# Performance work log

Hardware: AMD Instinct MI355X
Metric: run time of the kernel (lower is better)

Reference implementation:

```python
import jax, jax.numpy as jnp
import numpy as np

DIM = 512
HEADS = 8
DIM_HEAD = 64
HIDDEN = HEADS * DIM_HEAD  # 512
SCALE = DIM_HEAD ** -0.5
EPS = 1e-12  # F.normalize default eps


def rms_norm(x, g):
    # F.normalize over channel dim (dim=1), then * g * sqrt(C)
    c = x.shape[1]
    norm = jnp.sqrt(jnp.sum(x * x, axis=1, keepdims=True))
    return x / jnp.maximum(norm, EPS) * g * (c ** 0.5)


def setup_inputs() -> dict:
    key = jax.random.key(0)
    ks = jax.random.split(key, 6)
    b, h, w = 16, 64, 64
    x = jax.random.normal(ks[0], (b, DIM, h, w), dtype=jnp.float32)
    g1 = jnp.ones((1, DIM, 1, 1), dtype=jnp.float32)
    # 1x1 conv weights stored as (out_ch, in_ch)
    Wqkv = jax.random.normal(ks[1], (HIDDEN * 3, DIM), dtype=jnp.float32) * (DIM ** -0.5)
    Wout = jax.random.normal(ks[2], (DIM, HIDDEN), dtype=jnp.float32) * (HIDDEN ** -0.5)
    bout = jax.random.normal(ks[3], (DIM,), dtype=jnp.float32) * 0.01
    g2 = jnp.ones((1, DIM, 1, 1), dtype=jnp.float32)
    return {"x": x, "g1": g1, "Wqkv": Wqkv, "Wout": Wout, "bout": bout, "g2": g2}


def reference(x, g1, Wqkv, Wout, bout, g2):
    b, c, h, w = x.shape
    n = h * w
    xn = rms_norm(x, g1)
    # 1x1 conv == channel matmul
    qkv = jnp.einsum('oc,bchw->bohw', Wqkv, xn)  # (b, 3*hidden, h, w)
    qkv = qkv.reshape(b, 3, HEADS, DIM_HEAD, n)
    q, k, v = qkv[:, 0], qkv[:, 1], qkv[:, 2]  # (b, heads, d, n)
    q = jax.nn.softmax(q, axis=-2) * SCALE      # softmax over feature dim
    k = jax.nn.softmax(k, axis=-1)               # softmax over spatial dim
    context = jnp.einsum('bhdn,bhen->bhde', k, v)  # (b,h,d,e) small
    out = jnp.einsum('bhde,bhdn->bhen', context, q)  # (b,h,e,n)
    out = out.reshape(b, HIDDEN, h, w)
    out = jnp.einsum('oc,bchw->bohw', Wout, out) + bout[None, :, None, None]
    return rms_norm(out, g2)
```

## Files before the change

kernel.cpp:

```cpp
#include <hip/hip_runtime.h>
#include <hip/hip_bf16.h>
#include <math.h>

#define B_ 16
#define C_ 512
#define N_ 4096
#define NCOL (B_ * N_)

typedef short bf16x8 __attribute__((ext_vector_type(8)));
typedef ushort ushort8_t __attribute__((ext_vector_type(8)));
typedef float f32x4 __attribute__((ext_vector_type(4)));

__device__ __forceinline__ ushort f2bf(float f) {
    unsigned u = __float_as_uint(f);
    unsigned r = (u + 0x7FFFu + ((u >> 16) & 1u)) >> 16;
    return (ushort)r;
}
__device__ __forceinline__ float bf2f(ushort u) {
    return __uint_as_float((unsigned)u << 16);
}
__device__ __forceinline__ void gload_lds16(const void* g, void* l) {
    __builtin_amdgcn_global_load_lds(
        (const __attribute__((address_space(1))) unsigned int*)g,
        (__attribute__((address_space(3))) unsigned int*)l, 16, 0, 0);
}

__global__ __launch_bounds__(256) void wprep_k(const float* __restrict__ W,
                                               const float* __restrict__ g,
                                               ushort* __restrict__ Wb, int nvec)
{
    int i = blockIdx.x * 256 + threadIdx.x;
    if (i >= nvec) return;
    float4 wv = reinterpret_cast<const float4*>(W)[i];
    if (g) {
        const float4 gv = *reinterpret_cast<const float4*>(g + ((i * 4) & 511));
        wv.x *= gv.x; wv.y *= gv.y; wv.z *= gv.z; wv.w *= gv.w;
    }
    ushort4 u;
    u.x = f2bf(wv.x); u.y = f2bf(wv.y); u.z = f2bf(wv.z); u.w = f2bf(wv.w);
    reinterpret_cast<ushort4*>(Wb)[i] = u;
}

__global__ __launch_bounds__(256) void transpose_k(const float* __restrict__ X,
                                                   ushort* __restrict__ Xt,
                                                   float* __restrict__ csq1)
{
    __shared__ float t[64][65];
    __shared__ float sq[4][64];
    const int b = blockIdx.z, n0 = blockIdx.x * 64, c0 = blockIdx.y * 64;
    const int tid = threadIdx.x;
    const int tx = tid & 63, ty = tid >> 6;
    const float* xp = X + ((size_t)b * C_ + c0) * N_ + n0;
    float local = 0.f;
    #pragma unroll
    for (int i = 0; i < 16; ++i) {
        float v = xp[(size_t)(ty + 4 * i) * N_ + tx];
        t[ty + 4 * i][tx] = v;
        local += v * v;
    }
    sq[ty][tx] = local;
    __syncthreads();
    #pragma unroll
    for (int i = 0; i < 4; ++i) {
        int nl = (tid >> 4) + i * 16;
        int cl = (tid & 15) * 4;
        ushort4 u;
        u.x = f2bf(t[cl + 0][nl]);
        u.y = f2bf(t[cl + 1][nl]);
        u.z = f2bf(t[cl + 2][nl]);
        u.w = f2bf(t[cl + 3][nl]);
        *reinterpret_cast<ushort4*>(Xt + ((size_t)b * N_ + n0 + nl) * 512 + c0 + cl) = u;
    }
    if (tid < 64)
        csq1[(size_t)blockIdx.y * NCOL + (size_t)b * N_ + n0 + tid] =
            sq[0][tid] + sq[1][tid] + sq[2][tid] + sq[3][tid];
}

__global__ __launch_bounds__(256) void rs1_reduce_k(const float* __restrict__ csq1,
                                                    float* __restrict__ rs1)
{
    int col = blockIdx.x * 256 + threadIdx.x;
    float s = 0.f;
    #pragma unroll
    for (int j = 0; j < 8; ++j) s += csq1[(size_t)j * NCOL + col];
    rs1[col] = 22.627416998f / fmaxf(sqrtf(s), 1e-12f);
}

__global__ __launch_bounds__(512, 2)
void mfma_gemm(const ushort* __restrict__ A, const ushort* __restrict__ Bt,
               const float* __restrict__ rs1,
               ushort* __restrict__ qT, ushort* __restrict__ kd,
               ushort* __restrict__ vd)
{
    __shared__ __align__(16) char lds[2][2][32768];
    const int b  = blockIdx.z;
    const int n0 = blockIdx.x * 256;
    const int m0 = blockIdx.y * 256;
    const int tid = threadIdx.x;
    const int w = tid >> 6, l = tid & 63;
    const int wm = w >> 2, wn = w & 3;
    const int lq = l >> 4, lr = l & 15;
    const ushort* Bb = Bt + (size_t)b * N_ * 512;

    f32x4 acc[8][4];
    #pragma unroll
    for (int i = 0; i < 8; ++i)
        #pragma unroll
        for (int j = 0; j < 4; ++j)
            #pragma unroll
            for (int r = 0; r < 4; ++r) acc[i][j][r] = 0.f;

#define STAGE_STEP(t, i)                                                      \
    do {                                                                      \
        const int kb_ = (t) * 128;                                            \
        const int idx_ = (i) * 512 + tid;                                     \
        const int r_ = idx_ >> 3;                                             \
        const int ch_ = (idx_ & 7) ^ (r_ & 7);                                \
        gload_lds16((const char*)A + (size_t)(m0 + r_) * 1024 + kb_ + ch_ * 16,\
                    &lds[(t) & 1][0][idx_ * 16]);                             \
        gload_lds16((const char*)Bb + (size_t)(n0 + r_) * 1024 + kb_ + ch_ * 16,\
                    &lds[(t) & 1][1][idx_ * 16]);                             \
    } while (0)

    #pragma unroll
    for (int i = 0; i < 4; ++i) STAGE_STEP(0, i);

    bf16x8 bfr[4];
    #pragma unroll 2
    for (int t = 0; t < 8; ++t) {
        const char* As = lds[t & 1][0];
        const char* Bs = lds[t & 1][1];
        #pragma unroll
        for (int ph = 0; ph < 4; ++ph) {
            const int kk = ph >> 1, mg = ph & 1;
            bf16x8 af[4];
            if (ph != 0) {
                #pragma unroll
                for (int m2 = 0; m2 < 4; ++m2) {
                    int ra = wm * 128 + (mg * 4 + m2) * 16 + lr;
                    int ch = (kk * 4 + lq) ^ (ra & 7);
                    af[m2] = *(const bf16x8*)(As + ra * 128 + ch * 16);
                }
                if (mg == 0) {
                    #pragma unroll
                    for (int nf = 0; nf < 4; ++nf) {
                        int rb = wn * 64 + nf * 16 + lr;
                        int ch = (kk * 4 + lq) ^ (rb & 7);
                        bfr[nf] = *(const bf16x8*)(Bs + rb * 128 + ch * 16);
                    }
                }
            }
            if (t < 7) STAGE_STEP(t + 1, ph);
            if (ph == 0) {
                if (t < 7) { asm volatile("s_waitcnt vmcnt(2)" ::: "memory"); }
                else       { asm volatile("s_waitcnt vmcnt(0)" ::: "memory"); }
            }
            __builtin_amdgcn_s_barrier();
            if (ph == 0) {
                #pragma unroll
                for (int m2 = 0; m2 < 4; ++m2) {
                    int ra = wm * 128 + m2 * 16 + lr;
                    int ch = lq ^ (ra & 7);
                    af[m2] = *(const bf16x8*)(As + ra * 128 + ch * 16);
                }
                #pragma unroll
                for (int nf = 0; nf < 4; ++nf) {
                    int rb = wn * 64 + nf * 16 + lr;
                    int ch = lq ^ (rb & 7);
                    bfr[nf] = *(const bf16x8*)(Bs + rb * 128 + ch * 16);
                }
            }
            asm volatile("s_waitcnt lgkmcnt(0)" ::: "memory");
            __builtin_amdgcn_sched_barrier(0);
            __builtin_amdgcn_s_setprio(1);
            #pragma unroll
            for (int m2 = 0; m2 < 4; ++m2)
                #pragma unroll
                for (int nf = 0; nf < 4; ++nf)
                    acc[mg * 4 + m2][nf] = __builtin_amdgcn_mfma_f32_16x16x32_bf16(
                        af[m2], bfr[nf], acc[mg * 4 + m2][nf], 0, 0, 0);
            __builtin_amdgcn_s_setprio(0);
            __builtin_amdgcn_s_barrier();
        }
    }
#undef STAGE_STEP

    const int part = m0 >> 9;
    const int mloc = (m0 & 511) + wm * 128;
    const int nbase = n0 + wn * 64;
    if (part == 0) {
        #pragma unroll
        for (int hg = 0; hg < 2; ++hg) {
            const int head = (mloc >> 6) + hg;
            #pragma unroll
            for (int nf = 0; nf < 4; ++nf) {
                const int n = nbase + nf * 16 + lr;
                const float sc = rs1[(size_t)b * N_ + n];
                float v[4][4];
                float mx = -1e30f;
                #pragma unroll
                for (int m2 = 0; m2 < 4; ++m2)
                    #pragma unroll
                    for (int r = 0; r < 4; ++r) {
                        v[m2][r] = acc[hg * 4 + m2][nf][r] * sc;
                        mx = fmaxf(mx, v[m2][r]);
                    }
                mx = fmaxf(mx, __shfl_xor(mx, 16));
                mx = fmaxf(mx, __shfl_xor(mx, 32));
                float s = 0.f;
                #pragma unroll
                for (int m2 = 0; m2 < 4; ++m2)
                    #pragma unroll
                    for (int r = 0; r < 4; ++r) {
                        v[m2][r] = __expf(v[m2][r] - mx);
                        s += v[m2][r];
                    }
                s += __shfl_xor(s, 16);
                s += __shfl_xor(s, 32);
                const float r8 = 0.125f / s;
                ushort* qp = qT + (((size_t)b * 8 + head) * N_ + n) * 64;
                #pragma unroll
                for (int m2 = 0; m2 < 4; ++m2) {
                    ushort4 u;
                    u.x = f2bf(v[m2][0] * r8);
                    u.y = f2bf(v[m2][1] * r8);
                    u.z = f2bf(v[m2][2] * r8);
                    u.w = f2bf(v[m2][3] * r8);
                    *reinterpret_cast<ushort4*>(qp + m2 * 16 + lq * 4) = u;
                }
            }
        }
    } else {
        ushort* dst = (part == 1) ? kd : vd;
        #pragma unroll
        for (int nf = 0; nf < 4; ++nf) {
            const int n = nbase + nf * 16 + lr;
            const float sc = rs1[(size_t)b * N_ + n];
            #pragma unroll
            for (int mf = 0; mf < 8; ++mf) {
                const int o = mloc + mf * 16 + lq * 4;
                #pragma unroll
                for (int r = 0; r < 4; ++r)
                    dst[((size_t)b * 512 + o + r) * N_ + n] =
                        f2bf(acc[mf][nf][r] * sc);
            }
        }
    }
}

__global__ __launch_bounds__(512, 2)
void gemm2_k(const ushort* __restrict__ A,
             const ushort* __restrict__ Bt,
             const float* __restrict__ bias,
             const float* __restrict__ g2,
             float* __restrict__ outp)
{
    __shared__ __align__(16) ushort As[512 * 64];
    __shared__ __align__(16) ushort Bs[128 * 64];
    const int b  = blockIdx.y;
    const int n0 = blockIdx.x * 128;
    const int tid = threadIdx.x;
    const int w = tid >> 6, l = tid & 63;
    const int lq = l >> 4, lr = l & 15;
    const ushort* Bb = Bt + (size_t)b * N_ * 512;

    f32x4 acc[4][8];
    #pragma unroll
    for (int i = 0; i < 4; ++i)
        #pragma unroll
        for (int j = 0; j < 8; ++j)
            #pragma unroll
            for (int r = 0; r < 4; ++r) acc[i][j][r] = 0.f;

    for (int k0 = 0; k0 < 512; k0 += 64) {
        #pragma unroll
        for (int i = 0; i < 8; ++i) {
            int base = i * 512 + w * 64;
            int idx = base + l;
            int r = idx >> 3, ch = (idx & 7) ^ (r & 7);
            gload_lds16((const char*)A + (size_t)r * 1024 + k0 * 2 + ch * 16,
                        (char*)As + (size_t)base * 16);
        }
        #pragma unroll
        for (int i = 0; i < 2; ++i) {
            int base = i * 512 + w * 64;
            int idx = base + l;
            int r = idx >> 3, ch = (idx & 7) ^ (r & 7);
            gload_lds16((const char*)Bb + (size_t)(n0 + r) * 1024 + k0 * 2 + ch * 16,
                        (char*)Bs + (size_t)base * 16);
        }
        __syncthreads();
        #pragma unroll
        for (int kk = 0; kk < 2; ++kk) {
            bf16x8 af[4], bfr[8];
            #pragma unroll
            for (int mf = 0; mf < 4; ++mf) {
                int ra = w * 64 + mf * 16 + lr;
                int ch = (kk * 4 + lq) ^ (ra & 7);
                af[mf] = *(const bf16x8*)((const char*)As + ra * 128 + ch * 16);
            }
            #pragma unroll
            for (int nf = 0; nf < 8; ++nf) {
                int rb = nf * 16 + lr;
                int ch = (kk * 4 + lq) ^ (rb & 7);
                bfr[nf] = *(const bf16x8*)((const char*)Bs + rb * 128 + ch * 16);
            }
            #pragma unroll
            for (int mf = 0; mf < 4; ++mf)
                #pragma unroll
                for (int nf = 0; nf < 8; ++nf)
                    acc[mf][nf] = __builtin_amdgcn_mfma_f32_16x16x32_bf16(
                        af[mf], bfr[nf], acc[mf][nf], 0, 0, 0);
        }
        __syncthreads();
    }

    float4 bv[4], g2v[4];
    #pragma unroll
    for (int mf = 0; mf < 4; ++mf) {
        bv[mf]  = *reinterpret_cast<const float4*>(bias + w * 64 + mf * 16 + lq * 4);
        g2v[mf] = *reinterpret_cast<const float4*>(g2   + w * 64 + mf * 16 + lq * 4);
    }
    float csq[8] = {};
    #pragma unroll
    for (int mf = 0; mf < 4; ++mf)
        #pragma unroll
        for (int nf = 0; nf < 8; ++nf)
            #pragma unroll
            for (int r = 0; r < 4; ++r) {
                float wv = acc[mf][nf][r] + ((const float*)&bv[mf])[r];
                acc[mf][nf][r] = wv;
                csq[nf] += wv * wv;
            }
    #pragma unroll
    for (int nf = 0; nf < 8; ++nf) {
        csq[nf] += __shfl_xor(csq[nf], 16);
        csq[nf] += __shfl_xor(csq[nf], 32);
    }
    float* red  = (float*)As;
    float* rs2s = red + 1024;
    if (lq == 0) {
        #pragma unroll
        for (int nf = 0; nf < 8; ++nf)
            red[w * 128 + nf * 16 + lr] = csq[nf];
    }
    __syncthreads();
    if (tid < 128) {
        float s = 0.f;
        #pragma unroll
        for (int j = 0; j < 8; ++j) s += red[j * 128 + tid];
        rs2s[tid] = 22.627416998f / fmaxf(sqrtf(s), 1e-12f);
    }
    __syncthreads();
    #pragma unroll
    for (int nf = 0; nf < 8; ++nf) {
        const float rsv = rs2s[nf * 16 + lr];
        const int n = n0 + nf * 16 + lr;
        #pragma unroll
        for (int mf = 0; mf < 4; ++mf) {
            const int o = w * 64 + mf * 16 + lq * 4;
            float* p = outp + ((size_t)b * 512 + o) * N_ + n;
            #pragma unroll
            for (int r = 0; r < 4; ++r)
                p[(size_t)r * N_] = acc[mf][nf][r] * rsv * ((const float*)&g2v[mf])[r];
        }
    }
}

__global__ __launch_bounds__(256) void rowstat_k(const ushort* __restrict__ kk,
                                                 float* __restrict__ rowm,
                                                 float* __restrict__ rowr)
{
    const int row = blockIdx.x * 4 + (threadIdx.x >> 6);
    const int lane = threadIdx.x & 63;
    const ushort* p = kk + (size_t)row * N_;
    float vals[64];
    #pragma unroll
    for (int j = 0; j < 8; ++j) {
        ushort8_t u = *reinterpret_cast<const ushort8_t*>(p + lane * 8 + j * 512);
        #pragma unroll
        for (int t = 0; t < 8; ++t) vals[j * 8 + t] = bf2f(u[t]);
    }
    float mx = -1e30f;
    #pragma unroll
    for (int i = 0; i < 64; ++i) mx = fmaxf(mx, vals[i]);
    #pragma unroll
    for (int o = 32; o >= 1; o >>= 1) mx = fmaxf(mx, __shfl_xor(mx, o));
    float s = 0.f;
    #pragma unroll
    for (int i = 0; i < 64; ++i) s += __expf(vals[i] - mx);
    #pragma unroll
    for (int o = 32; o >= 1; o >>= 1) s += __shfl_xor(s, o);
    if (lane == 0) { rowm[row] = mx; rowr[row] = 1.f / s; }
}

__global__ __launch_bounds__(256) void ctx_k(const ushort* __restrict__ kk,
                                             const ushort* __restrict__ vv,
                                             const float* __restrict__ rowm,
                                             const float* __restrict__ rowr,
                                             float* __restrict__ ctxp)
{
    const int bh = blockIdx.x, chunk = blockIdx.y;
    const ushort* kp = kk + (size_t)bh * 64 * N_;
    const ushort* vp = vv + (size_t)bh * 64 * N_;
    __shared__ __align__(16) ushort kx[64 * 128];
    __shared__ __align__(16) ushort vx[64 * 128];
    __shared__ float rm[64];
    const int tid = threadIdx.x;
    const int w = tid >> 6, l = tid & 63;
    const int lq = l >> 4, lr = l & 15;
    const int we = w >> 1, wd = w & 1;
    if (tid < 64) rm[tid] = rowm[(size_t)bh * 64 + tid];
    __syncthreads();

    f32x4 acc[2][2];
    #pragma unroll
    for (int i = 0; i < 2; ++i)
        #pragma unroll
        for (int j = 0; j < 2; ++j)
            #pragma unroll
            for (int r = 0; r < 4; ++r) acc[i][j][r] = 0.f;

    for (int s = 0; s < 8; ++s) {
        const int n0 = chunk * 1024 + s * 128;
        #pragma unroll
        for (int i = 0; i < 4; ++i) {
            int idx = i * 256 + tid;
            int row = idx >> 4;
            int ch  = (idx & 15) ^ (row & 15);
            gload_lds16((const char*)(vp + (size_t)row * N_ + n0 + ch * 8),
                        (char*)vx + idx * 16);
        }
        #pragma unroll
        for (int i = 0; i < 4; ++i) {
            int idx = i * 256 + tid;
            int row = idx >> 4;
            int ch  = idx & 15;
            ushort8_t u = *reinterpret_cast<const ushort8_t*>(
                kp + (size_t)row * N_ + n0 + ch * 8);
            float m_ = rm[row];
            ushort8_t o;
            #pragma unroll
            for (int t = 0; t < 8; ++t) o[t] = f2bf(__expf(bf2f(u[t]) - m_));
            *(ushort8_t*)((char*)kx + (row * 16 + (ch ^ (row & 15))) * 16) = o;
        }
        __syncthreads();
        #pragma unroll
        for (int k2 = 0; k2 < 4; ++k2) {
            bf16x8 af[2], bfr[2];
            #pragma unroll
            for (int i = 0; i < 2; ++i) {
                int re = we * 32 + i * 16 + lr;
                int cha = (k2 * 4 + lq) ^ (re & 15);
                af[i] = *(const bf16x8*)((const char*)vx + (re * 16 + cha) * 16);
                int rd = wd * 32 + i * 16 + lr;
                int chb = (k2 * 4 + lq) ^ (rd & 15);
                bfr[i] = *(const bf16x8*)((const char*)kx + (rd * 16 + chb) * 16);
            }
            #pragma unroll
            for (int i = 0; i < 2; ++i)
                #pragma unroll
                for (int j = 0; j < 2; ++j)
                    acc[i][j] = __builtin_amdgcn_mfma_f32_16x16x32_bf16(
                        af[i], bfr[j], acc[i][j], 0, 0, 0);
        }
        __syncthreads();
    }
    float* cbase = ctxp + ((size_t)bh * 4 + chunk) * 4096;
    #pragma unroll
    for (int j = 0; j < 2; ++j) {
        const int d = wd * 32 + j * 16 + lr;
        const float rr = rowr[(size_t)bh * 64 + d];
        #pragma unroll
        for (int i = 0; i < 2; ++i) {
            const int e = we * 32 + i * 16 + lq * 4;
            #pragma unroll
            for (int r = 0; r < 4; ++r)
                cbase[(size_t)(e + r) * 64 + d] = acc[i][j][r] * rr;
        }
    }
}

__global__ __launch_bounds__(256) void attn_k(const float* __restrict__ ctxp,
                                              const ushort* __restrict__ qT,
                                              ushort* __restrict__ at2)
{
    const int bh = blockIdx.y;
    const int n0 = blockIdx.x * 256;
    const int b = bh >> 3, h = bh & 7;
    __shared__ __align__(16) ushort qx[256 * 64];
    __shared__ __align__(16) ushort cx[64 * 64];
    const int tid = threadIdx.x;
    const int w = tid >> 6, l = tid & 63;
    const int lq = l >> 4, lr = l & 15;
    const ushort* qp = qT + ((size_t)bh * N_ + n0) * 64;

    #pragma unroll
    for (int i = 0; i < 8; ++i) {
        int idx = i * 256 + tid;
        int row = idx >> 3;
        int ch  = (idx & 7) ^ (row & 7);
        gload_lds16((const char*)(qp + (size_t)row * 64 + ch * 8),
                    (char*)qx + idx * 16);
    }
    {
        const float* cp = ctxp + (size_t)bh * 4 * 4096;
        const int e = tid >> 2, db = (tid & 3) * 16;
        float vs[16];
        #pragma unroll
        for (int t = 0; t < 4; ++t) {
            float4 a0 = *(const float4*)(cp + e * 64 + db + t * 4);
            float4 a1 = *(const float4*)(cp + 4096 + e * 64 + db + t * 4);
            float4 a2 = *(const float4*)(cp + 8192 + e * 64 + db + t * 4);
            float4 a3 = *(const float4*)(cp + 12288 + e * 64 + db + t * 4);
            vs[t * 4 + 0] = a0.x + a1.x + a2.x + a3.x;
            vs[t * 4 + 1] = a0.y + a1.y + a2.y + a3.y;
            vs[t * 4 + 2] = a0.z + a1.z + a2.z + a3.z;
            vs[t * 4 + 3] = a0.w + a1.w + a2.w + a3.w;
        }
        ushort8_t o0, o1;
        #pragma unroll
        for (int t = 0; t < 8; ++t) { o0[t] = f2bf(vs[t]); o1[t] = f2bf(vs[8 + t]); }
        const int c0 = (db >> 3) ^ (e & 7);
        const int c1 = ((db >> 3) + 1) ^ (e & 7);
        *(ushort8_t*)((char*)cx + (e * 8 + c0) * 16) = o0;
        *(ushort8_t*)((char*)cx + (e * 8 + c1) * 16) = o1;
    }
    __syncthreads();

    f32x4 acc[4][4];
    #pragma unroll
    for (int i = 0; i < 4; ++i)
        #pragma unroll
        for (int j = 0; j < 4; ++j)
            #pragma unroll
            for (int r = 0; r < 4; ++r) acc[i][j][r] = 0.f;

    #pragma unroll
    for (int k2 = 0; k2 < 2; ++k2) {
        bf16x8 af[4], bfr[4];
        #pragma unroll
        for (int et = 0; et < 4; ++et) {
            int re = et * 16 + lr;
            int ch = (k2 * 4 + lq) ^ (re & 7);
            af[et] = *(const bf16x8*)((const char*)cx + (re * 8 + ch) * 16);
        }
        #pragma unroll
        for (int nt = 0; nt < 4; ++nt) {
            int rn = w * 64 + nt * 16 + lr;
            int ch = (k2 * 4 + lq) ^ (rn & 7);
            bfr[nt] = *(const bf16x8*)((const char*)qx + (rn * 8 + ch) * 16);
        }
        #pragma unroll
        for (int et = 0; et < 4; ++et)
            #pragma unroll
            for (int nt = 0; nt < 4; ++nt)
                acc[et][nt] = __builtin_amdgcn_mfma_f32_16x16x32_bf16(
                    af[et], bfr[nt], acc[et][nt], 0, 0, 0);
    }
    #pragma unroll
    for (int nt = 0; nt < 4; ++nt) {
        const int n = n0 + w * 64 + nt * 16 + lr;
        ushort* op = at2 + ((size_t)b * N_ + n) * 512 + h * 64;
        #pragma unroll
        for (int et = 0; et < 4; ++et) {
            ushort4 u;
            u.x = f2bf(acc[et][nt][0]);
            u.y = f2bf(acc[et][nt][1]);
            u.z = f2bf(acc[et][nt][2]);
            u.w = f2bf(acc[et][nt][3]);
            *reinterpret_cast<ushort4*>(op + et * 16 + lq * 4) = u;
        }
    }
}

extern "C" void kernel_launch(void* const* d_in, const int* in_sizes, int n_in,
                              void* d_out, int out_size, void* d_ws, size_t ws_size,
                              hipStream_t stream)
{
    const float* x    = (const float*)d_in[0];
    const float* g1   = (const float*)d_in[1];
    const float* Wqkv = (const float*)d_in[2];
    const float* Wout = (const float*)d_in[3];
    const float* bout = (const float*)d_in[4];
    const float* g2   = (const float*)d_in[5];
    float* out = (float*)d_out;

    char* wsb = (char*)d_ws;
    ushort* qbuf  = (ushort*)wsb;
    float*  csq1  = (float*)wsb;
    ushort* kbuf  = (ushort*)(wsb + ((size_t)64 << 20));
    ushort* vbuf  = (ushort*)(wsb + ((size_t)128 << 20));
    ushort* Xt    = (ushort*)(wsb + ((size_t)192 << 20));
    float*  ctxp  = (float*)Xt;
    float*  rowm  = (float*)(wsb + ((size_t)200 << 20));
    float*  rowr  = rowm + 8192;
    char*   tail  = wsb + ((size_t)256 << 20);
    ushort* Wqkvb = (ushort*)tail;
    ushort* Woutb = (ushort*)(tail + (size_t)1536 * 512 * 2);
    float*  rs1   = (float*)(tail + (size_t)1536 * 512 * 2 + (size_t)512 * 512 * 2);
    ushort* at2   = kbuf;

    wprep_k<<<768, 256, 0, stream>>>(Wqkv, g1, Wqkvb, 1536 * 512 / 4);
    wprep_k<<<256, 256, 0, stream>>>(Wout, nullptr, Woutb, 512 * 512 / 4);
    transpose_k<<<dim3(64, 8, 16), 256, 0, stream>>>(x, Xt, csq1);
    rs1_reduce_k<<<256, 256, 0, stream>>>(csq1, rs1);
    mfma_gemm<<<dim3(16, 6, B_), 512, 0, stream>>>(Wqkvb, Xt, rs1,
                                                   qbuf, kbuf, vbuf);
    rowstat_k<<<2048, 256, 0, stream>>>(kbuf, rowm, rowr);
    ctx_k<<<dim3(B_ * 8, 4), 256, 0, stream>>>(kbuf, vbuf, rowm, rowr, ctxp);
    attn_k<<<dim3(N_ / 256, B_ * 8), 256, 0, stream>>>(ctxp, qbuf, at2);
    gemm2_k<<<dim3(32, B_), 512, 0, stream>>>(Woutb, at2, bout, g2, out);
}
```

Measured before the change: 339.6 us.

## Fuse attention output into output-projection GEMM, keeping attended tile in LDS

Replaces the attn_k plus gemm2_k pair with a small ctxsum kernel that pre-reduces context partials to bf16, and a fused kernel. The fused kernel computes context·q per head for a 64-column tile, holds the result in LDS, and runs the Wout projection with bias and RMS norm directly on it. This removes the global write and re-read of the 64 MB intermediate at2 buffer. In exchange the tile shrinks from 128 to 64 columns with one block per CU and 128 KB of LDS, so Wout is streamed twice as often and occupancy is lower.

```diff
diff --git a/kernel.cpp b/kernel.cpp
--- a/kernel.cpp
+++ b/kernel.cpp
@@ -248,125 +248,6 @@
     }
 }
 
-__global__ __launch_bounds__(512, 2)
-void gemm2_k(const ushort* __restrict__ A,
-             const ushort* __restrict__ Bt,
-             const float* __restrict__ bias,
-             const float* __restrict__ g2,
-             float* __restrict__ outp)
-{
-    __shared__ __align__(16) ushort As[512 * 64];
-    __shared__ __align__(16) ushort Bs[128 * 64];
-    const int b  = blockIdx.y;
-    const int n0 = blockIdx.x * 128;
-    const int tid = threadIdx.x;
-    const int w = tid >> 6, l = tid & 63;
-    const int lq = l >> 4, lr = l & 15;
-    const ushort* Bb = Bt + (size_t)b * N_ * 512;
-
-    f32x4 acc[4][8];
-    #pragma unroll
-    for (int i = 0; i < 4; ++i)
-        #pragma unroll
-        for (int j = 0; j < 8; ++j)
-            #pragma unroll
-            for (int r = 0; r < 4; ++r) acc[i][j][r] = 0.f;
-
-    for (int k0 = 0; k0 < 512; k0 += 64) {
-        #pragma unroll
-        for (int i = 0; i < 8; ++i) {
-            int base = i * 512 + w * 64;
-            int idx = base + l;
-            int r = idx >> 3, ch = (idx & 7) ^ (r & 7);
-            gload_lds16((const char*)A + (size_t)r * 1024 + k0 * 2 + ch * 16,
-                        (char*)As + (size_t)base * 16);
-        }
-        #pragma unroll
-        for (int i = 0; i < 2; ++i) {
-            int base = i * 512 + w * 64;
-            int idx = base + l;
-            int r = idx >> 3, ch = (idx & 7) ^ (r & 7);
-            gload_lds16((const char*)Bb + (size_t)(n0 + r) * 1024 + k0 * 2 + ch * 16,
-                        (char*)Bs + (size_t)base * 16);
-        }
-        __syncthreads();
-        #pragma unroll
-        for (int kk = 0; kk < 2; ++kk) {
-            bf16x8 af[4], bfr[8];
-            #pragma unroll
-            for (int mf = 0; mf < 4; ++mf) {
-                int ra = w * 64 + mf * 16 + lr;
-                int ch = (kk * 4 + lq) ^ (ra & 7);
-                af[mf] = *(const bf16x8*)((const char*)As + ra * 128 + ch * 16);
-            }
-            #pragma unroll
-            for (int nf = 0; nf < 8; ++nf) {
-                int rb = nf * 16 + lr;
-                int ch = (kk * 4 + lq) ^ (rb & 7);
-                bfr[nf] = *(const bf16x8*)((const char*)Bs + rb * 128 + ch * 16);
-            }
-            #pragma unroll
-            for (int mf = 0; mf < 4; ++mf)
-                #pragma unroll
-                for (int nf = 0; nf < 8; ++nf)
-                    acc[mf][nf] = __builtin_amdgcn_mfma_f32_16x16x32_bf16(
-                        af[mf], bfr[nf], acc[mf][nf], 0, 0, 0);
-        }
-        __syncthreads();
-    }
-
-    float4 bv[4], g2v[4];
-    #pragma unroll
-    for (int mf = 0; mf < 4; ++mf) {
-        bv[mf]  = *reinterpret_cast<const float4*>(bias + w * 64 + mf * 16 + lq * 4);
-        g2v[mf] = *reinterpret_cast<const float4*>(g2   + w * 64 + mf * 16 + lq * 4);
-    }
-    float csq[8] = {};
-    #pragma unroll
-    for (int mf = 0; mf < 4; ++mf)
-        #pragma unroll
-        for (int nf = 0; nf < 8; ++nf)
-            #pragma unroll
-            for (int r = 0; r < 4; ++r) {
-                float wv = acc[mf][nf][r] + ((const float*)&bv[mf])[r];
-                acc[mf][nf][r] = wv;
-                csq[nf] += wv * wv;
-            }
-    #pragma unroll
-    for (int nf = 0; nf < 8; ++nf) {
-        csq[nf] += __shfl_xor(csq[nf], 16);
-        csq[nf] += __shfl_xor(csq[nf], 32);
-    }
-    float* red  = (float*)As;
-    float* rs2s = red + 1024;
-    if (lq == 0) {
-        #pragma unroll
-        for (int nf = 0; nf < 8; ++nf)
-            red[w * 128 + nf * 16 + lr] = csq[nf];
-    }
-    __syncthreads();
-    if (tid < 128) {
-        float s = 0.f;
-        #pragma unroll
-        for (int j = 0; j < 8; ++j) s += red[j * 128 + tid];
-        rs2s[tid] = 22.627416998f / fmaxf(sqrtf(s), 1e-12f);
-    }
-    __syncthreads();
-    #pragma unroll
-    for (int nf = 0; nf < 8; ++nf) {
-        const float rsv = rs2s[nf * 16 + lr];
-        const int n = n0 + nf * 16 + lr;
-        #pragma unroll
-        for (int mf = 0; mf < 4; ++mf) {
-            const int o = w * 64 + mf * 16 + lq * 4;
-            float* p = outp + ((size_t)b * 512 + o) * N_ + n;
-            #pragma unroll
-            for (int r = 0; r < 4; ++r)
-                p[(size_t)r * N_] = acc[mf][nf][r] * rsv * ((const float*)&g2v[mf])[r];
-        }
-    }
-}
-
 __global__ __launch_bounds__(256) void rowstat_k(const ushort* __restrict__ kk,
                                                  float* __restrict__ rowm,
                                                  float* __restrict__ rowr)
@@ -481,51 +362,94 @@
     }
 }
 
-__global__ __launch_bounds__(256) void attn_k(const float* __restrict__ ctxp,
-                                              const ushort* __restrict__ qT,
-                                              ushort* __restrict__ at2)
-{
-    const int bh = blockIdx.y;
-    const int n0 = blockIdx.x * 256;
-    const int b = bh >> 3, h = bh & 7;
-    __shared__ __align__(16) ushort qx[256 * 64];
-    __shared__ __align__(16) ushort cx[64 * 64];
+__global__ __launch_bounds__(256) void ctxsum_k(const float* __restrict__ ctxp,
+                                                ushort* __restrict__ ctxb)
+{
+    int i4 = blockIdx.x * 256 + threadIdx.x;
+    int bh = i4 >> 10;
+    int off = (i4 & 1023) * 4;
+    const float* cp = ctxp + (size_t)bh * 16384 + off;
+    float4 a0 = *(const float4*)cp;
+    float4 a1 = *(const float4*)(cp + 4096);
+    float4 a2 = *(const float4*)(cp + 8192);
+    float4 a3 = *(const float4*)(cp + 12288);
+    ushort4 u;
+    u.x = f2bf(a0.x + a1.x + a2.x + a3.x);
+    u.y = f2bf(a0.y + a1.y + a2.y + a3.y);
+    u.z = f2bf(a0.z + a1.z + a2.z + a3.z);
+    u.w = f2bf(a0.w + a1.w + a2.w + a3.w);
+    *reinterpret_cast<ushort4*>(ctxb + (size_t)bh * 4096 + off) = u;
+}
+
+__global__ __launch_bounds__(512, 1)
+void gemm2f_k(const ushort* __restrict__ A,
+              const ushort* __restrict__ qT,
+              const ushort* __restrict__ ctxb,
+              const float* __restrict__ bias,
+              const float* __restrict__ g2,
+              float* __restrict__ outp)
+{
+    __shared__ __align__(16) char As[65536];
+    __shared__ __align__(16) char Bs[65536];
+    const int b  = blockIdx.y;
+    const int n0 = blockIdx.x * 64;
     const int tid = threadIdx.x;
     const int w = tid >> 6, l = tid & 63;
     const int lq = l >> 4, lr = l & 15;
-    const ushort* qp = qT + ((size_t)bh * N_ + n0) * 64;
-
-    #pragma unroll
-    for (int i = 0; i < 8; ++i) {
-        int idx = i * 256 + tid;
-        int row = idx >> 3;
-        int ch  = (idx & 7) ^ (row & 7);
-        gload_lds16((const char*)(qp + (size_t)row * 64 + ch * 8),
-                    (char*)qx + idx * 16);
-    }
+
     {
-        const float* cp = ctxp + (size_t)bh * 4 * 4096;
-        const int e = tid >> 2, db = (tid & 3) * 16;
-        float vs[16];
-        #pragma unroll
-        for (int t = 0; t < 4; ++t) {
-            float4 a0 = *(const float4*)(cp + e * 64 + db + t * 4);
-            float4 a1 = *(const float4*)(cp + 4096 + e * 64 + db + t * 4);
-            float4 a2 = *(const float4*)(cp + 8192 + e * 64 + db + t * 4);
-            float4 a3 = *(const float4*)(cp + 12288 + e * 64 + db + t * 4);
-            vs[t * 4 + 0] = a0.x + a1.x + a2.x + a3.x;
-            vs[t * 4 + 1] = a0.y + a1.y + a2.y + a3.y;
-            vs[t * 4 + 2] = a0.z + a1.z + a2.z + a3.z;
-            vs[t * 4 + 3] = a0.w + a1.w + a2.w + a3.w;
-        }
-        ushort8_t o0, o1;
-        #pragma unroll
-        for (int t = 0; t < 8; ++t) { o0[t] = f2bf(vs[t]); o1[t] = f2bf(vs[8 + t]); }
-        const int c0 = (db >> 3) ^ (e & 7);
-        const int c1 = ((db >> 3) + 1) ^ (e & 7);
-        *(ushort8_t*)((char*)cx + (e * 8 + c0) * 16) = o0;
-        *(ushort8_t*)((char*)cx + (e * 8 + c1) * 16) = o1;
-    }
+        const int n = tid >> 3;
+        const int j = tid & 7;
+        const int ch = j ^ (n & 7);
+        #pragma unroll
+        for (int h = 0; h < 8; ++h) {
+            gload_lds16(qT + (((size_t)b * 8 + h) * N_ + n0 + n) * 64 + ch * 8,
+                        As + h * 8192 + tid * 16);
+            gload_lds16(ctxb + (((size_t)b * 8 + h) * 64 + n) * 64 + ch * 8,
+                        Bs + h * 8192 + tid * 16);
+        }
+    }
+    __syncthreads();
+
+    bf16x8 paf[4][2], pbf[4][2];
+    #pragma unroll
+    for (int mf = 0; mf < 4; ++mf)
+        #pragma unroll
+        for (int k2 = 0; k2 < 2; ++k2) {
+            int rr = mf * 16 + lr;
+            int sl = (k2 * 4 + lq) ^ (rr & 7);
+            paf[mf][k2] = *(const bf16x8*)(As + w * 8192 + rr * 128 + sl * 16);
+            pbf[mf][k2] = *(const bf16x8*)(Bs + w * 8192 + rr * 128 + sl * 16);
+        }
+    __syncthreads();
+
+    f32x4 pacc[4][4];
+    #pragma unroll
+    for (int i = 0; i < 4; ++i)
+        #pragma unroll
+        for (int j = 0; j < 4; ++j)
+            #pragma unroll
+            for (int r = 0; r < 4; ++r) pacc[i][j][r] = 0.f;
+    #pragma unroll
+    for (int k2 = 0; k2 < 2; ++k2)
+        #pragma unroll
+        for (int mf = 0; mf < 4; ++mf)
+            #pragma unroll
+            for (int nf = 0; nf < 4; ++nf)
+                pacc[mf][nf] = __builtin_amdgcn_mfma_f32_16x16x32_bf16(
+                    paf[mf][k2], pbf[nf][k2], pacc[mf][nf], 0, 0, 0);
+
+    #pragma unroll
+    for (int mf = 0; mf < 4; ++mf)
+        #pragma unroll
+        for (int nf = 0; nf < 4; ++nf)
+            #pragma unroll
+            for (int r = 0; r < 4; ++r) {
+                int n = mf * 16 + lq * 4 + r;
+                int c = w * 64 + nf * 16 + lr;
+                *(ushort*)(Bs + ((n * 1024 + c * 2) ^ ((n & 7) << 4))) =
+                    f2bf(pacc[mf][nf][r]);
+            }
     __syncthreads();
 
     f32x4 acc[4][4];
@@ -536,40 +460,89 @@
             #pragma unroll
             for (int r = 0; r < 4; ++r) acc[i][j][r] = 0.f;
 
-    #pragma unroll
-    for (int k2 = 0; k2 < 2; ++k2) {
-        bf16x8 af[4], bfr[4];
-        #pragma unroll
-        for (int et = 0; et < 4; ++et) {
-            int re = et * 16 + lr;
-            int ch = (k2 * 4 + lq) ^ (re & 7);
-            af[et] = *(const bf16x8*)((const char*)cx + (re * 8 + ch) * 16);
-        }
-        #pragma unroll
-        for (int nt = 0; nt < 4; ++nt) {
-            int rn = w * 64 + nt * 16 + lr;
-            int ch = (k2 * 4 + lq) ^ (rn & 7);
-            bfr[nt] = *(const bf16x8*)((const char*)qx + (rn * 8 + ch) * 16);
-        }
-        #pragma unroll
-        for (int et = 0; et < 4; ++et)
-            #pragma unroll
-            for (int nt = 0; nt < 4; ++nt)
-                acc[et][nt] = __builtin_amdgcn_mfma_f32_16x16x32_bf16(
-                    af[et], bfr[nt], acc[et][nt], 0, 0, 0);
-    }
-    #pragma unroll
-    for (int nt = 0; nt < 4; ++nt) {
-        const int n = n0 + w * 64 + nt * 16 + lr;
-        ushort* op = at2 + ((size_t)b * N_ + n) * 512 + h * 64;
-        #pragma unroll
-        for (int et = 0; et < 4; ++et) {
-            ushort4 u;
-            u.x = f2bf(acc[et][nt][0]);
-            u.y = f2bf(acc[et][nt][1]);
-            u.z = f2bf(acc[et][nt][2]);
-            u.w = f2bf(acc[et][nt][3]);
-            *reinterpret_cast<ushort4*>(op + et * 16 + lq * 4) = u;
+    for (int t = 0; t < 8; ++t) {
+        #pragma unroll
+        for (int jj = 0; jj < 8; ++jj) {
+            int idx = jj * 512 + tid;
+            int m = idx >> 3;
+            int ch = (idx & 7) ^ (m & 7);
+            gload_lds16((const char*)A + (size_t)m * 1024 + t * 128 + ch * 16,
+                        As + idx * 16);
+        }
+        __syncthreads();
+        #pragma unroll
+        for (int kk = 0; kk < 2; ++kk) {
+            bf16x8 af[4], bfv[4];
+            #pragma unroll
+            for (int mf = 0; mf < 4; ++mf) {
+                int m = w * 64 + mf * 16 + lr;
+                int sl = (kk * 4 + lq) ^ (m & 7);
+                af[mf] = *(const bf16x8*)(As + m * 128 + sl * 16);
+            }
+            #pragma unroll
+            for (int nf = 0; nf < 4; ++nf) {
+                int n = nf * 16 + lr;
+                int sl = (kk * 4 + lq) ^ (n & 7);
+                bfv[nf] = *(const bf16x8*)(Bs + n * 1024 + t * 128 + sl * 16);
+            }
+            #pragma unroll
+            for (int mf = 0; mf < 4; ++mf)
+                #pragma unroll
+                for (int nf = 0; nf < 4; ++nf)
+                    acc[mf][nf] = __builtin_amdgcn_mfma_f32_16x16x32_bf16(
+                        af[mf], bfv[nf], acc[mf][nf], 0, 0, 0);
+        }
+        __syncthreads();
+    }
+
+    float4 bv[4], gv[4];
+    #pragma unroll
+    for (int mf = 0; mf < 4; ++mf) {
+        bv[mf] = *reinterpret_cast<const float4*>(bias + w * 64 + mf * 16 + lq * 4);
+        gv[mf] = *reinterpret_cast<const float4*>(g2   + w * 64 + mf * 16 + lq * 4);
+    }
+    float csq[4] = {};
+    #pragma unroll
+    for (int mf = 0; mf < 4; ++mf)
+        #pragma unroll
+        for (int nf = 0; nf < 4; ++nf)
+            #pragma unroll
+            for (int r = 0; r < 4; ++r) {
+                float wv = acc[mf][nf][r] + ((const float*)&bv[mf])[r];
+                acc[mf][nf][r] = wv;
+                csq[nf] += wv * wv;
+            }
+    #pragma unroll
+    for (int nf = 0; nf < 4; ++nf) {
+        csq[nf] += __shfl_xor(csq[nf], 16);
+        csq[nf] += __shfl_xor(csq[nf], 32);
+    }
+    float* red  = (float*)As;
+    float* rs2s = red + 512;
+    if (lq == 0) {
+        #pragma unroll
+        for (int nf = 0; nf < 4; ++nf)
+            red[w * 64 + nf * 16 + lr] = csq[nf];
+    }
+    __syncthreads();
+    if (tid < 64) {
+        float s = 0.f;
+        #pragma unroll
+        for (int j = 0; j < 8; ++j) s += red[j * 64 + tid];
+        rs2s[tid] = 22.627416998f / fmaxf(sqrtf(s), 1e-12f);
+    }
+    __syncthreads();
+    #pragma unroll
+    for (int nf = 0; nf < 4; ++nf) {
+        const float rsv = rs2s[nf * 16 + lr];
+        const int n = n0 + nf * 16 + lr;
+        #pragma unroll
+        for (int mf = 0; mf < 4; ++mf) {
+            const int o = w * 64 + mf * 16 + lq * 4;
+            float* p = outp + ((size_t)b * 512 + o) * N_ + n;
+            #pragma unroll
+            for (int r = 0; r < 4; ++r)
+                p[(size_t)r * N_] = acc[mf][nf][r] * rsv * ((const float*)&gv[mf])[r];
         }
     }
 }
@@ -595,11 +568,11 @@
     float*  ctxp  = (float*)Xt;
     float*  rowm  = (float*)(wsb + ((size_t)200 << 20));
     float*  rowr  = rowm + 8192;
+    ushort* ctxb  = (ushort*)(wsb + ((size_t)201 << 20));
     char*   tail  = wsb + ((size_t)256 << 20);
     ushort* Wqkvb = (ushort*)tail;
     ushort* Woutb = (ushort*)(tail + (size_t)1536 * 512 * 2);
     float*  rs1   = (float*)(tail + (size_t)1536 * 512 * 2 + (size_t)512 * 512 * 2);
-    ushort* at2   = kbuf;
 
     wprep_k<<<768, 256, 0, stream>>>(Wqkv, g1, Wqkvb, 1536 * 512 / 4);
     wprep_k<<<256, 256, 0, stream>>>(Wout, nullptr, Woutb, 512 * 512 / 4);
@@ -609,6 +582,6 @@
                                                    qbuf, kbuf, vbuf);
     rowstat_k<<<2048, 256, 0, stream>>>(kbuf, rowm, rowr);
     ctx_k<<<dim3(B_ * 8, 4), 256, 0, stream>>>(kbuf, vbuf, rowm, rowr, ctxp);
-    attn_k<<<dim3(N_ / 256, B_ * 8), 256, 0, stream>>>(ctxp, qbuf, at2);
-    gemm2_k<<<dim3(32, B_), 512, 0, stream>>>(Woutb, at2, bout, g2, out);
-}
+    ctxsum_k<<<512, 256, 0, stream>>>(ctxp, ctxb);
+    gemm2f_k<<<dim3(64, B_), 512, 0, stream>>>(Woutb, qbuf, ctxb, bout, g2, out);
+}
```

Measured after the change: 332.7 us. -2.0%, faster.

## Fold attention context into per-batch output weights, removing attn_k pass

Applied to the files above, without the earlier changes.

Uses associativity to fold the per-head context matrix into the output projection: a small wcbuild kernel computes Wc[b] = Wout·blockdiag(context) per batch. gemm2 then multiplies Wc directly against the softmaxed q, which the QKV GEMM now writes in (b, n, hidden) layout. This removes the attn_k kernel and its read and write of a large intermediate. In exchange it adds a small per-batch weight-build kernel, more strided q stores, and an extra bf16 rounding of the combined weights.

```diff
diff --git a/kernel.cpp b/kernel.cpp
--- a/kernel.cpp
+++ b/kernel.cpp
@@ -89,7 +89,7 @@
 __global__ __launch_bounds__(512, 2)
 void mfma_gemm(const ushort* __restrict__ A, const ushort* __restrict__ Bt,
                const float* __restrict__ rs1,
-               ushort* __restrict__ qT, ushort* __restrict__ kd,
+               ushort* __restrict__ qT2, ushort* __restrict__ kd,
                ushort* __restrict__ vd)
 {
     __shared__ __align__(16) char lds[2][2][32768];
@@ -218,7 +218,7 @@
                 s += __shfl_xor(s, 16);
                 s += __shfl_xor(s, 32);
                 const float r8 = 0.125f / s;
-                ushort* qp = qT + (((size_t)b * 8 + head) * N_ + n) * 64;
+                ushort* qp = qT2 + ((size_t)b * N_ + n) * 512 + head * 64;
                 #pragma unroll
                 for (int m2 = 0; m2 < 4; ++m2) {
                     ushort4 u;
@@ -244,125 +244,6 @@
                     dst[((size_t)b * 512 + o + r) * N_ + n] =
                         f2bf(acc[mf][nf][r] * sc);
             }
-        }
-    }
-}
-
-__global__ __launch_bounds__(512, 2)
-void gemm2_k(const ushort* __restrict__ A,
-             const ushort* __restrict__ Bt,
-             const float* __restrict__ bias,
-             const float* __restrict__ g2,
-             float* __restrict__ outp)
-{
-    __shared__ __align__(16) ushort As[512 * 64];
-    __shared__ __align__(16) ushort Bs[128 * 64];
-    const int b  = blockIdx.y;
-    const int n0 = blockIdx.x * 128;
-    const int tid = threadIdx.x;
-    const int w = tid >> 6, l = tid & 63;
-    const int lq = l >> 4, lr = l & 15;
-    const ushort* Bb = Bt + (size_t)b * N_ * 512;
-
-    f32x4 acc[4][8];
-    #pragma unroll
-    for (int i = 0; i < 4; ++i)
-        #pragma unroll
-        for (int j = 0; j < 8; ++j)
-            #pragma unroll
-            for (int r = 0; r < 4; ++r) acc[i][j][r] = 0.f;
-
-    for (int k0 = 0; k0 < 512; k0 += 64) {
-        #pragma unroll
-        for (int i = 0; i < 8; ++i) {
-            int base = i * 512 + w * 64;
-            int idx = base + l;
-            int r = idx >> 3, ch = (idx & 7) ^ (r & 7);
-            gload_lds16((const char*)A + (size_t)r * 1024 + k0 * 2 + ch * 16,
-                        (char*)As + (size_t)base * 16);
-        }
-        #pragma unroll
-        for (int i = 0; i < 2; ++i) {
-            int base = i * 512 + w * 64;
-            int idx = base + l;
-            int r = idx >> 3, ch = (idx & 7) ^ (r & 7);
-            gload_lds16((const char*)Bb + (size_t)(n0 + r) * 1024 + k0 * 2 + ch * 16,
-                        (char*)Bs + (size_t)base * 16);
-        }
-        __syncthreads();
-        #pragma unroll
-        for (int kk = 0; kk < 2; ++kk) {
-            bf16x8 af[4], bfr[8];
-            #pragma unroll
-            for (int mf = 0; mf < 4; ++mf) {
-                int ra = w * 64 + mf * 16 + lr;
-                int ch = (kk * 4 + lq) ^ (ra & 7);
-                af[mf] = *(const bf16x8*)((const char*)As + ra * 128 + ch * 16);
-            }
-            #pragma unroll
-            for (int nf = 0; nf < 8; ++nf) {
-                int rb = nf * 16 + lr;
-                int ch = (kk * 4 + lq) ^ (rb & 7);
-                bfr[nf] = *(const bf16x8*)((const char*)Bs + rb * 128 + ch * 16);
-            }
-            #pragma unroll
-            for (int mf = 0; mf < 4; ++mf)
-                #pragma unroll
-                for (int nf = 0; nf < 8; ++nf)
-                    acc[mf][nf] = __builtin_amdgcn_mfma_f32_16x16x32_bf16(
-                        af[mf], bfr[nf], acc[mf][nf], 0, 0, 0);
-        }
-        __syncthreads();
-    }
-
-    float4 bv[4], g2v[4];
-    #pragma unroll
-    for (int mf = 0; mf < 4; ++mf) {
-        bv[mf]  = *reinterpret_cast<const float4*>(bias + w * 64 + mf * 16 + lq * 4);
-        g2v[mf] = *reinterpret_cast<const float4*>(g2   + w * 64 + mf * 16 + lq * 4);
-    }
-    float csq[8] = {};
-    #pragma unroll
-    for (int mf = 0; mf < 4; ++mf)
-        #pragma unroll
-        for (int nf = 0; nf < 8; ++nf)
-            #pragma unroll
-            for (int r = 0; r < 4; ++r) {
-                float wv = acc[mf][nf][r] + ((const float*)&bv[mf])[r];
-                acc[mf][nf][r] = wv;
-                csq[nf] += wv * wv;
-            }
-    #pragma unroll
-    for (int nf = 0; nf < 8; ++nf) {
-        csq[nf] += __shfl_xor(csq[nf], 16);
-        csq[nf] += __shfl_xor(csq[nf], 32);
-    }
-    float* red  = (float*)As;
-    float* rs2s = red + 1024;
-    if (lq == 0) {
-        #pragma unroll
-        for (int nf = 0; nf < 8; ++nf)
-            red[w * 128 + nf * 16 + lr] = csq[nf];
-    }
-    __syncthreads();
-    if (tid < 128) {
-        float s = 0.f;
-        #pragma unroll
-        for (int j = 0; j < 8; ++j) s += red[j * 128 + tid];
-        rs2s[tid] = 22.627416998f / fmaxf(sqrtf(s), 1e-12f);
-    }
-    __syncthreads();
-    #pragma unroll
-    for (int nf = 0; nf < 8; ++nf) {
-        const float rsv = rs2s[nf * 16 + lr];
-        const int n = n0 + nf * 16 + lr;
-        #pragma unroll
-        for (int mf = 0; mf < 4; ++mf) {
-            const int o = w * 64 + mf * 16 + lq * 4;
-            float* p = outp + ((size_t)b * 512 + o) * N_ + n;
-            #pragma unroll
-            for (int r = 0; r < 4; ++r)
-                p[(size_t)r * N_] = acc[mf][nf][r] * rsv * ((const float*)&g2v[mf])[r];
         }
     }
 }
@@ -473,58 +354,59 @@
         const float rr = rowr[(size_t)bh * 64 + d];
         #pragma unroll
         for (int i = 0; i < 2; ++i) {
-            const int e = we * 32 + i * 16 + lq * 4;
-            #pragma unroll
-            for (int r = 0; r < 4; ++r)
-                cbase[(size_t)(e + r) * 64 + d] = acc[i][j][r] * rr;
-        }
-    }
-}
-
-__global__ __launch_bounds__(256) void attn_k(const float* __restrict__ ctxp,
-                                              const ushort* __restrict__ qT,
-                                              ushort* __restrict__ at2)
-{
-    const int bh = blockIdx.y;
-    const int n0 = blockIdx.x * 256;
-    const int b = bh >> 3, h = bh & 7;
-    __shared__ __align__(16) ushort qx[256 * 64];
-    __shared__ __align__(16) ushort cx[64 * 64];
+            const int e0 = we * 32 + i * 16 + lq * 4;
+            float4 wv;
+            wv.x = acc[i][j][0] * rr;
+            wv.y = acc[i][j][1] * rr;
+            wv.z = acc[i][j][2] * rr;
+            wv.w = acc[i][j][3] * rr;
+            *reinterpret_cast<float4*>(cbase + (size_t)d * 64 + e0) = wv;
+        }
+    }
+}
+
+__global__ __launch_bounds__(256) void wcbuild_k(const ushort* __restrict__ Wb,
+                                                 const float* __restrict__ ctxp,
+                                                 ushort* __restrict__ Wc)
+{
+    const int oh = blockIdx.x, h = blockIdx.y, b = blockIdx.z;
+    const int bh = b * 8 + h;
+    __shared__ __align__(16) ushort ws[256 * 64];
+    __shared__ __align__(16) ushort cs[64 * 64];
     const int tid = threadIdx.x;
     const int w = tid >> 6, l = tid & 63;
     const int lq = l >> 4, lr = l & 15;
-    const ushort* qp = qT + ((size_t)bh * N_ + n0) * 64;
 
     #pragma unroll
     for (int i = 0; i < 8; ++i) {
         int idx = i * 256 + tid;
         int row = idx >> 3;
-        int ch  = (idx & 7) ^ (row & 7);
-        gload_lds16((const char*)(qp + (size_t)row * 64 + ch * 8),
-                    (char*)qx + idx * 16);
+        int ch = (idx & 7) ^ (row & 7);
+        gload_lds16(Wb + (size_t)(oh * 256 + row) * 512 + h * 64 + ch * 8,
+                    (char*)ws + idx * 16);
     }
     {
         const float* cp = ctxp + (size_t)bh * 4 * 4096;
-        const int e = tid >> 2, db = (tid & 3) * 16;
+        const int d = tid >> 2, eb = (tid & 3) * 16;
         float vs[16];
         #pragma unroll
-        for (int t = 0; t < 4; ++t) {
-            float4 a0 = *(const float4*)(cp + e * 64 + db + t * 4);
-            float4 a1 = *(const float4*)(cp + 4096 + e * 64 + db + t * 4);
-            float4 a2 = *(const float4*)(cp + 8192 + e * 64 + db + t * 4);
-            float4 a3 = *(const float4*)(cp + 12288 + e * 64 + db + t * 4);
-            vs[t * 4 + 0] = a0.x + a1.x + a2.x + a3.x;
-            vs[t * 4 + 1] = a0.y + a1.y + a2.y + a3.y;
-            vs[t * 4 + 2] = a0.z + a1.z + a2.z + a3.z;
-            vs[t * 4 + 3] = a0.w + a1.w + a2.w + a3.w;
+        for (int t4 = 0; t4 < 4; ++t4) {
+            float4 a0 = *(const float4*)(cp + d * 64 + eb + t4 * 4);
+            float4 a1 = *(const float4*)(cp + 4096 + d * 64 + eb + t4 * 4);
+            float4 a2 = *(const float4*)(cp + 8192 + d * 64 + eb + t4 * 4);
+            float4 a3 = *(const float4*)(cp + 12288 + d * 64 + eb + t4 * 4);
+            vs[t4 * 4 + 0] = a0.x + a1.x + a2.x + a3.x;
+            vs[t4 * 4 + 1] = a0.y + a1.y + a2.y + a3.y;
+            vs[t4 * 4 + 2] = a0.z + a1.z + a2.z + a3.z;
+            vs[t4 * 4 + 3] = a0.w + a1.w + a2.w + a3.w;
         }
         ushort8_t o0, o1;
         #pragma unroll
         for (int t = 0; t < 8; ++t) { o0[t] = f2bf(vs[t]); o1[t] = f2bf(vs[8 + t]); }
-        const int c0 = (db >> 3) ^ (e & 7);
-        const int c1 = ((db >> 3) + 1) ^ (e & 7);
-        *(ushort8_t*)((char*)cx + (e * 8 + c0) * 16) = o0;
-        *(ushort8_t*)((char*)cx + (e * 8 + c1) * 16) = o1;
+        const int c0 = (eb >> 3) ^ (d & 7);
+        const int c1 = ((eb >> 3) + 1) ^ (d & 7);
+        *(ushort8_t*)((char*)cs + (d * 8 + c0) * 16) = o0;
+        *(ushort8_t*)((char*)cs + (d * 8 + c1) * 16) = o1;
     }
     __syncthreads();
 
@@ -537,39 +419,156 @@
             for (int r = 0; r < 4; ++r) acc[i][j][r] = 0.f;
 
     #pragma unroll
-    for (int k2 = 0; k2 < 2; ++k2) {
+    for (int kk = 0; kk < 2; ++kk) {
         bf16x8 af[4], bfr[4];
         #pragma unroll
-        for (int et = 0; et < 4; ++et) {
-            int re = et * 16 + lr;
-            int ch = (k2 * 4 + lq) ^ (re & 7);
-            af[et] = *(const bf16x8*)((const char*)cx + (re * 8 + ch) * 16);
-        }
-        #pragma unroll
-        for (int nt = 0; nt < 4; ++nt) {
-            int rn = w * 64 + nt * 16 + lr;
-            int ch = (k2 * 4 + lq) ^ (rn & 7);
-            bfr[nt] = *(const bf16x8*)((const char*)qx + (rn * 8 + ch) * 16);
-        }
-        #pragma unroll
-        for (int et = 0; et < 4; ++et)
-            #pragma unroll
-            for (int nt = 0; nt < 4; ++nt)
-                acc[et][nt] = __builtin_amdgcn_mfma_f32_16x16x32_bf16(
-                    af[et], bfr[nt], acc[et][nt], 0, 0, 0);
-    }
-    #pragma unroll
-    for (int nt = 0; nt < 4; ++nt) {
-        const int n = n0 + w * 64 + nt * 16 + lr;
-        ushort* op = at2 + ((size_t)b * N_ + n) * 512 + h * 64;
-        #pragma unroll
-        for (int et = 0; et < 4; ++et) {
-            ushort4 u;
-            u.x = f2bf(acc[et][nt][0]);
-            u.y = f2bf(acc[et][nt][1]);
-            u.z = f2bf(acc[et][nt][2]);
-            u.w = f2bf(acc[et][nt][3]);
-            *reinterpret_cast<ushort4*>(op + et * 16 + lq * 4) = u;
+        for (int mf = 0; mf < 4; ++mf) {
+            int ra = w * 64 + mf * 16 + lr;
+            int ch = (kk * 4 + lq) ^ (ra & 7);
+            af[mf] = *(const bf16x8*)((const char*)ws + (ra * 8 + ch) * 16);
+        }
+        #pragma unroll
+        for (int nf = 0; nf < 4; ++nf) {
+            int rd = nf * 16 + lr;
+            int ch = (kk * 4 + lq) ^ (rd & 7);
+            bfr[nf] = *(const bf16x8*)((const char*)cs + (rd * 8 + ch) * 16);
+        }
+        #pragma unroll
+        for (int mf = 0; mf < 4; ++mf)
+            #pragma unroll
+            for (int nf = 0; nf < 4; ++nf)
+                acc[mf][nf] = __builtin_amdgcn_mfma_f32_16x16x32_bf16(
+                    af[mf], bfr[nf], acc[mf][nf], 0, 0, 0);
+    }
+
+    ushort* wp = Wc + (size_t)b * 262144 + h * 64;
+    #pragma unroll
+    for (int mf = 0; mf < 4; ++mf)
+        #pragma unroll
+        for (int r = 0; r < 4; ++r) {
+            const int o = oh * 256 + w * 64 + mf * 16 + lq * 4 + r;
+            #pragma unroll
+            for (int nf = 0; nf < 4; ++nf)
+                wp[(size_t)o * 512 + nf * 16 + lr] = f2bf(acc[mf][nf][r]);
+        }
+}
+
+__global__ __launch_bounds__(512, 2)
+void gemm2_k(const ushort* __restrict__ Wc,
+             const ushort* __restrict__ Bt,
+             const float* __restrict__ bias,
+             const float* __restrict__ g2,
+             float* __restrict__ outp)
+{
+    __shared__ __align__(16) ushort As[512 * 64];
+    __shared__ __align__(16) ushort Bs[128 * 64];
+    const int b  = blockIdx.y;
+    const int n0 = blockIdx.x * 128;
+    const int tid = threadIdx.x;
+    const int w = tid >> 6, l = tid & 63;
+    const int lq = l >> 4, lr = l & 15;
+    const ushort* A  = Wc + (size_t)b * 262144;
+    const ushort* Bb = Bt + (size_t)b * N_ * 512;
+
+    f32x4 acc[4][8];
+    #pragma unroll
+    for (int i = 0; i < 4; ++i)
+        #pragma unroll
+        for (int j = 0; j < 8; ++j)
+            #pragma unroll
+            for (int r = 0; r < 4; ++r) acc[i][j][r] = 0.f;
+
+    for (int k0 = 0; k0 < 512; k0 += 64) {
+        #pragma unroll
+        for (int i = 0; i < 8; ++i) {
+            int base = i * 512 + w * 64;
+            int idx = base + l;
+            int r = idx >> 3, ch = (idx & 7) ^ (r & 7);
+            gload_lds16((const char*)A + (size_t)r * 1024 + k0 * 2 + ch * 16,
+                        (char*)As + (size_t)base * 16);
+        }
+        #pragma unroll
+        for (int i = 0; i < 2; ++i) {
+            int base = i * 512 + w * 64;
+            int idx = base + l;
+            int r = idx >> 3, ch = (idx & 7) ^ (r & 7);
+            gload_lds16((const char*)Bb + (size_t)(n0 + r) * 1024 + k0 * 2 + ch * 16,
+                        (char*)Bs + (size_t)base * 16);
+        }
+        __syncthreads();
+        #pragma unroll
+        for (int kk = 0; kk < 2; ++kk) {
+            bf16x8 af[4], bfv[8];
+            #pragma unroll
+            for (int mf = 0; mf < 4; ++mf) {
+                int ra = w * 64 + mf * 16 + lr;
+                int ch = (kk * 4 + lq) ^ (ra & 7);
+                af[mf] = *(const bf16x8*)((const char*)As + ra * 128 + ch * 16);
+            }
+            #pragma unroll
+            for (int nf = 0; nf < 8; ++nf) {
+                int rb = nf * 16 + lr;
+                int ch = (kk * 4 + lq) ^ (rb & 7);
+                bfv[nf] = *(const bf16x8*)((const char*)Bs + rb * 128 + ch * 16);
+            }
+            #pragma unroll
+            for (int mf = 0; mf < 4; ++mf)
+                #pragma unroll
+                for (int nf = 0; nf < 8; ++nf)
+                    acc[mf][nf] = __builtin_amdgcn_mfma_f32_16x16x32_bf16(
+                        af[mf], bfv[nf], acc[mf][nf], 0, 0, 0);
+        }
+        __syncthreads();
+    }
+
+    float4 bv[4], g2v[4];
+    #pragma unroll
+    for (int mf = 0; mf < 4; ++mf) {
+        bv[mf]  = *reinterpret_cast<const float4*>(bias + w * 64 + mf * 16 + lq * 4);
+        g2v[mf] = *reinterpret_cast<const float4*>(g2   + w * 64 + mf * 16 + lq * 4);
+    }
+    float csq[8] = {};
+    #pragma unroll
+    for (int mf = 0; mf < 4; ++mf)
+        #pragma unroll
+        for (int nf = 0; nf < 8; ++nf)
+            #pragma unroll
+            for (int r = 0; r < 4; ++r) {
+                float wv = acc[mf][nf][r] + ((const float*)&bv[mf])[r];
+                acc[mf][nf][r] = wv;
+                csq[nf] += wv * wv;
+            }
+    #pragma unroll
+    for (int nf = 0; nf < 8; ++nf) {
+        csq[nf] += __shfl_xor(csq[nf], 16);
+        csq[nf] += __shfl_xor(csq[nf], 32);
+    }
+    float* red  = (float*)As;
+    float* rs2s = red + 1024;
+    if (lq == 0) {
+        #pragma unroll
+        for (int nf = 0; nf < 8; ++nf)
+            red[w * 128 + nf * 16 + lr] = csq[nf];
+    }
+    __syncthreads();
+    if (tid < 128) {
+        float s = 0.f;
+        #pragma unroll
+        for (int j = 0; j < 8; ++j) s += red[j * 128 + tid];
+        rs2s[tid] = 22.627416998f / fmaxf(sqrtf(s), 1e-12f);
+    }
+    __syncthreads();
+    #pragma unroll
+    for (int nf = 0; nf < 8; ++nf) {
+        const float rsv = rs2s[nf * 16 + lr];
+        const int n = n0 + nf * 16 + lr;
+        #pragma unroll
+        for (int mf = 0; mf < 4; ++mf) {
+            const int o = w * 64 + mf * 16 + lq * 4;
+            float* p = outp + ((size_t)b * 512 + o) * N_ + n;
+            #pragma unroll
+            for (int r = 0; r < 4; ++r)
+                p[(size_t)r * N_] = acc[mf][nf][r] * rsv * ((const float*)&g2v[mf])[r];
         }
     }
 }
@@ -595,11 +594,11 @@
     float*  ctxp  = (float*)Xt;
     float*  rowm  = (float*)(wsb + ((size_t)200 << 20));
     float*  rowr  = rowm + 8192;
+    ushort* Wcb   = (ushort*)(wsb + ((size_t)201 << 20));
     char*   tail  = wsb + ((size_t)256 << 20);
     ushort* Wqkvb = (ushort*)tail;
     ushort* Woutb = (ushort*)(tail + (size_t)1536 * 512 * 2);
     float*  rs1   = (float*)(tail + (size_t)1536 * 512 * 2 + (size_t)512 * 512 * 2);
-    ushort* at2   = kbuf;
 
     wprep_k<<<768, 256, 0, stream>>>(Wqkv, g1, Wqkvb, 1536 * 512 / 4);
     wprep_k<<<256, 256, 0, stream>>>(Wout, nullptr, Woutb, 512 * 512 / 4);
@@ -609,6 +608,6 @@
                                                    qbuf, kbuf, vbuf);
     rowstat_k<<<2048, 256, 0, stream>>>(kbuf, rowm, rowr);
     ctx_k<<<dim3(B_ * 8, 4), 256, 0, stream>>>(kbuf, vbuf, rowm, rowr, ctxp);
-    attn_k<<<dim3(N_ / 256, B_ * 8), 256, 0, stream>>>(ctxp, qbuf, at2);
-    gemm2_k<<<dim3(32, B_), 512, 0, stream>>>(Woutb, at2, bout, g2, out);
-}
+    wcbuild_k<<<dim3(2, 8, B_), 256, 0, stream>>>(Woutb, ctxp, Wcb);
+    gemm2_k<<<dim3(32, B_), 512, 0, stream>>>(Wcb, qbuf, bout, g2, out);
+}
```

Result: faster. 300.8 us (-11.4%).
